# Performance work log

Hardware: AMD Instinct MI355X
Metric: run time of the kernel (lower is better)

Reference implementation:

```python
import jax, jax.numpy as jnp
import numpy as np

B, T, E, H = 2, 2048, 1024, 16
STD = 0.02

def setup_inputs() -> dict:
    key = jax.random.key(0)
    k1, k2, k3 = jax.random.split(key, 3)
    return {
        'x': jax.random.normal(k1, (B, T, E), dtype=jnp.float32),
        'mask': jnp.ones((B, T), dtype=bool),
        'w_attn': jax.random.normal(k2, (E, 3 * E), dtype=jnp.float32) * STD,
        'b_attn': jnp.zeros((3 * E,), dtype=jnp.float32),
        'w_proj': jax.random.normal(k3, (E, E), dtype=jnp.float32) * STD,
        'b_proj': jnp.zeros((E,), dtype=jnp.float32),
    }

def reference(x, mask, w_attn, b_attn, w_proj, b_proj):
    b, t, e = x.shape
    h = H
    hd = e // h  # head_dim
    qkv = x @ w_attn + b_attn                       # [B,T,3E]
    q, k, v = jnp.split(qkv, 3, axis=-1)
    q = q.reshape(b, t, h, hd).transpose(0, 2, 1, 3)  # [B,H,T,hd]
    k = k.reshape(b, t, h, hd).transpose(0, 2, 1, 3)
    v = v.reshape(b, t, h, hd).transpose(0, 2, 1, 3)
    scale = jnp.asarray(hd, dtype=x.dtype) ** (-0.5)
    scores = jnp.einsum('bnth,bnsh->bnts', q, k) * scale  # [B,H,T,T]
    causal = jnp.tril(jnp.ones((t, t), dtype=bool))
    full_mask = causal[None, None, :, :] & mask.astype(bool)[:, None, None, :]
    neg = jnp.asarray(jnp.finfo(x.dtype).min, dtype=x.dtype)
    bias = jnp.where(full_mask, jnp.asarray(0.0, dtype=x.dtype), neg)
    attn = jax.nn.softmax(scores + bias, axis=-1)
    out = jnp.einsum('bnts,bnsh->bnth', attn, v)    # [B,H,T,hd]
    out = out.transpose(0, 2, 1, 3).reshape(b, t, e)
    return out @ w_proj + b_proj
```

## Files before the change

### kernel.cpp

```cpp
#include <hip/hip_runtime.h>

typedef float f32x4 __attribute__((ext_vector_type(4)));
typedef float f32x16 __attribute__((ext_vector_type(16)));
typedef __bf16 bf16x8 __attribute__((ext_vector_type(8)));
typedef unsigned short ushort8_t __attribute__((ext_vector_type(8)));
typedef unsigned short ushort4_t __attribute__((ext_vector_type(4)));

#define GAS(p) ((const __attribute__((address_space(1))) void*)(p))
#define LAS(p) ((__attribute__((address_space(3))) void*)(p))

__device__ inline unsigned short f2bf(float f) {
    union { float f; unsigned int u; } v; v.f = f;
    unsigned int r = v.u + 0x7FFFu + ((v.u >> 16) & 1u);
    return (unsigned short)(r >> 16);
}

__device__ inline bf16x8 ld16(const unsigned short* p) {
    uint4 v = *reinterpret_cast<const uint4*>(p);
    return __builtin_bit_cast(bf16x8, v);
}

__device__ inline unsigned int cvtpk(float a, float b) {
    unsigned int r;
    asm("v_cvt_pk_bf16_f32 %0, %1, %2" : "=v"(r) : "v"(a), "v"(b));
    return r;
}

__device__ inline float swap_max(float x) { return fmaxf(x, __shfl_xor(x, 32)); }
__device__ inline float swap_add(float x) { return x + __shfl_xor(x, 32); }

__global__ __launch_bounds__(256) void k_f32_to_bf16(const float* __restrict__ x,
                                                     unsigned short* __restrict__ y, int n) {
    int i = (blockIdx.x * 256 + threadIdx.x) * 8;
    if (i >= n) return;
    float4 a = *reinterpret_cast<const float4*>(x + i);
    float4 b = *reinterpret_cast<const float4*>(x + i + 4);
    ushort8_t o;
    o[0]=f2bf(a.x); o[1]=f2bf(a.y); o[2]=f2bf(a.z); o[3]=f2bf(a.w);
    o[4]=f2bf(b.x); o[5]=f2bf(b.y); o[6]=f2bf(b.z); o[7]=f2bf(b.w);
    *reinterpret_cast<ushort8_t*>(y + i) = o;
}

__global__ __launch_bounds__(256) void k_transpose_bf16(const float* __restrict__ W,
                                                        unsigned short* __restrict__ WT,
                                                        int K, int N) {
    __shared__ unsigned short tile[64][72];
    int n0 = blockIdx.x * 64, k0 = blockIdx.y * 64;
    int tid = threadIdx.x;
    int r = tid >> 2;
    int c0 = (tid & 3) * 16;
    const float* src = W + (size_t)(k0 + r) * N + n0 + c0;
    #pragma unroll
    for (int i = 0; i < 4; ++i) {
        float4 v = reinterpret_cast<const float4*>(src)[i];
        tile[r][c0 + i*4 + 0] = f2bf(v.x);
        tile[r][c0 + i*4 + 1] = f2bf(v.y);
        tile[r][c0 + i*4 + 2] = f2bf(v.z);
        tile[r][c0 + i*4 + 3] = f2bf(v.w);
    }
    __syncthreads();
    unsigned short tmp[16];
    #pragma unroll
    for (int i = 0; i < 16; ++i) tmp[i] = tile[c0 + i][r];
    unsigned short* dst = WT + (size_t)(n0 + r) * K + k0 + c0;
    ushort8_t o0, o1;
    #pragma unroll
    for (int i = 0; i < 8; ++i) { o0[i] = tmp[i]; o1[i] = tmp[8 + i]; }
    *reinterpret_cast<ushort8_t*>(dst) = o0;
    *reinterpret_cast<ushort8_t*>(dst + 8) = o1;
}

template<int MODE>
__global__ __launch_bounds__(256) void k_gemm(const unsigned short* __restrict__ A,
                                              const unsigned short* __restrict__ BT,
                                              const float* __restrict__ bias,
                                              unsigned short* __restrict__ qo,
                                              unsigned short* __restrict__ ko,
                                              unsigned short* __restrict__ vo,
                                              float* __restrict__ outp,
                                              int K, int N) {
    __shared__ unsigned short As[128 * 32];
    __shared__ unsigned short Bs[128 * 32];
    int tid = threadIdx.x;
    int lane = tid & 63;
    int wave = tid >> 6;
    int wm = wave >> 1, wn = wave & 1;
    int bm = blockIdx.x * 128;
    int bn = blockIdx.y * 128;
    int r15 = lane & 15, g = lane >> 4;

    f32x4 acc[4][4];
    #pragma unroll
    for (int i = 0; i < 4; ++i)
        #pragma unroll
        for (int j = 0; j < 4; ++j)
            acc[i][j] = (f32x4){0.f, 0.f, 0.f, 0.f};

    for (int k0 = 0; k0 < K; k0 += 32) {
        #pragma unroll
        for (int it = 0; it < 2; ++it) {
            int ci = it * 256 + tid;
            int row = ci >> 2, cj = ci & 3;
            const unsigned short* ga = A + (size_t)(bm + row) * K + k0 + cj * 8;
            __builtin_amdgcn_global_load_lds(GAS(ga), LAS(As + (it * 256 + wave * 64) * 8), 16, 0, 0);
            const unsigned short* gb = BT + (size_t)(bn + row) * K + k0 + cj * 8;
            __builtin_amdgcn_global_load_lds(GAS(gb), LAS(Bs + (it * 256 + wave * 64) * 8), 16, 0, 0);
        }
        __syncthreads();
        bf16x8 af[4], bfr[4];
        #pragma unroll
        for (int i = 0; i < 4; ++i) af[i] = ld16(As + (wm * 64 + i * 16 + r15) * 32 + g * 8);
        #pragma unroll
        for (int j = 0; j < 4; ++j) bfr[j] = ld16(Bs + (wn * 64 + j * 16 + r15) * 32 + g * 8);
        #pragma unroll
        for (int i = 0; i < 4; ++i)
            #pragma unroll
            for (int j = 0; j < 4; ++j)
                acc[i][j] = __builtin_amdgcn_mfma_f32_16x16x32_bf16(af[i], bfr[j], acc[i][j], 0, 0, 0);
        __syncthreads();
    }

    const float QSCL = 0.18033688011112042f;
    #pragma unroll
    for (int i = 0; i < 4; ++i)
        #pragma unroll
        for (int j = 0; j < 4; ++j) {
            int col = bn + wn * 64 + j * 16 + r15;
            float bcol = bias[col];
            int row0 = bm + wm * 64 + i * 16 + g * 4;
            if (MODE == 0) {
                int which = col >> 10;
                int e = col & 1023;
                int hh = e >> 6, d = e & 63;
                int bb = row0 >> 11, t0 = row0 & 2047;
                size_t headbase = (size_t)(bb * 16 + hh) * 131072;
                if (which == 2) {
                    int blk = (t0 >> 2) & 3;
                    int t0p = (t0 & ~15) | ((((blk & 1) << 1) | (blk >> 1)) << 2);
                    int tilev = t0p >> 6, s6 = t0p & 63;
                    int sbv = s6 >> 5, s5 = s6 & 31;
                    int ksv = s5 >> 4, hiv = (s5 >> 3) & 1, jb = s5 & 7;
                    int dbv = d >> 5, lanev = hiv * 32 + (d & 31);
                    ushort4_t pk;
                    #pragma unroll
                    for (int rg = 0; rg < 4; ++rg) pk[rg] = f2bf(acc[i][j][rg] + bcol);
                    *reinterpret_cast<ushort4_t*>(vo + headbase +
                        (size_t)((((tilev * 2 + dbv) * 2 + sbv) * 2 + ksv) * 64 + lanev) * 8 + jb) = pk;
                } else {
                    unsigned short* dst = (which == 0) ? qo : ko;
                    float scl = (which == 0) ? QSCL : 1.0f;
                    int grp = t0 >> 5, l31q = t0 & 31;
                    int kbq = d >> 4, hiq = (d >> 3) & 1, jq = d & 7;
                    size_t base = headbase + (size_t)(grp * 4 + kbq) * 512 + hiq * 256 + l31q * 8 + jq;
                    #pragma unroll
                    for (int rg = 0; rg < 4; ++rg)
                        dst[base + rg * 8] = f2bf((acc[i][j][rg] + bcol) * scl);
                }
            } else {
                #pragma unroll
                for (int rg = 0; rg < 4; ++rg)
                    outp[(size_t)(row0 + rg) * 1024 + col] = acc[i][j][rg] + bcol;
            }
        }
}

#define ATTN_HALF(QF, OACC, MM, LL, TR, S0M, MASKED)                           \
  {                                                                            \
    f32x16 sacc[2];                                                            \
    _Pragma("unroll")                                                          \
    for (int sb = 0; sb < 2; ++sb)                                             \
      _Pragma("unroll")                                                        \
      for (int r = 0; r < 16; ++r) sacc[sb][r] = 0.f;                          \
    _Pragma("unroll")                                                          \
    for (int sb = 0; sb < 2; ++sb)                                             \
      _Pragma("unroll")                                                        \
      for (int kb = 0; kb < 4; ++kb)                                           \
        sacc[sb] = __builtin_amdgcn_mfma_f32_32x32x16_bf16(kf[sb][kb], QF[kb], sacc[sb], 0, 0, 0); \
    if (MASKED) {                                                              \
      _Pragma("unroll")                                                        \
      for (int sb = 0; sb < 2; ++sb)                                           \
        _Pragma("unroll")                                                      \
        for (int r = 0; r < 16; ++r) {                                         \
          int srw = (S0M) + sb * 32 + (r & 3) + 8 * (r >> 2) + 4 * hi;         \
          if (srw > (TR)) sacc[sb][r] = -3.0e38f;                              \
        }                                                                      \
    }                                                                          \
    float mt = sacc[0][0];                                                     \
    _Pragma("unroll")                                                          \
    for (int sb = 0; sb < 2; ++sb)                                             \
      _Pragma("unroll")                                                        \
      for (int r = 0; r < 16; ++r) mt = fmaxf(mt, sacc[sb][r]);                \
    mt = swap_max(mt);                                                         \
    if (__any(mt > MM + 8.f)) {                                                \
      float mnew = fmaxf(MM, mt);                                              \
      float alpha = exp2f(MM - mnew);                                          \
      MM = mnew;                                                               \
      LL *= alpha;                                                             \
      _Pragma("unroll")                                                        \
      for (int db = 0; db < 2; ++db)                                           \
        _Pragma("unroll")                                                      \
        for (int r = 0; r < 16; ++r) OACC[db][r] *= alpha;                     \
    }                                                                          \
    float rs = 0.f;                                                            \
    _Pragma("unroll")                                                          \
    for (int sb = 0; sb < 2; ++sb)                                             \
      _Pragma("unroll")                                                        \
      for (int r = 0; r < 16; ++r) {                                           \
        float p = exp2f(sacc[sb][r] - MM);                                     \
        sacc[sb][r] = p;                                                       \
        rs += p;                                                               \
      }                                                                        \
    LL += swap_add(rs);                                                        \
    _Pragma("unroll")                                                          \
    for (int sb = 0; sb < 2; ++sb) {                                           \
      bf16x8 pa[2];                                                            \
      _Pragma("unroll")                                                        \
      for (int ks = 0; ks < 2; ++ks) {                                         \
        int base = ks * 8;                                                     \
        uint4 u;                                                               \
        u.x = cvtpk(sacc[sb][base + 0], sacc[sb][base + 1]);                   \
        u.y = cvtpk(sacc[sb][base + 2], sacc[sb][base + 3]);                   \
        u.z = cvtpk(sacc[sb][base + 4], sacc[sb][base + 5]);                   \
        u.w = cvtpk(sacc[sb][base + 6], sacc[sb][base + 7]);                   \
        pa[ks] = __builtin_bit_cast(bf16x8, u);                                \
      }                                                                        \
      _Pragma("unroll")                                                        \
      for (int db = 0; db < 2; ++db)                                           \
        _Pragma("unroll")                                                      \
        for (int ks = 0; ks < 2; ++ks)                                         \
          OACC[db] = __builtin_amdgcn_mfma_f32_32x32x16_bf16(vf[db][sb][ks], pa[ks], OACC[db], 0, 0, 0); \
    }                                                                          \
  }

#define ATTN_TILE(S0, MASKED)                                                  \
  {                                                                            \
    int s0_ = (S0);                                                            \
    int tg_ = s0_ >> 5;                                                        \
    bf16x8 kf[2][4];                                                           \
    _Pragma("unroll")                                                          \
    for (int sb = 0; sb < 2; ++sb)                                             \
      _Pragma("unroll")                                                        \
      for (int kb = 0; kb < 4; ++kb)                                           \
        kf[sb][kb] = ld16(Kfb + (size_t)((tg_ + sb) * 4 + kb) * 512 + lane * 8); \
    int vt_ = s0_ >> 6;                                                        \
    bf16x8 vf[2][2][2];                                                        \
    _Pragma("unroll")                                                          \
    for (int db = 0; db < 2; ++db)                                             \
      _Pragma("unroll")                                                        \
      for (int sb = 0; sb < 2; ++sb)                                           \
        _Pragma("unroll")                                                      \
        for (int ks = 0; ks < 2; ++ks)                                         \
          vf[db][sb][ks] = ld16(Vfb + (size_t)(((vt_ * 2 + db) * 2 + sb) * 2 + ks) * 512 + lane * 8); \
    ATTN_HALF(qfA, oaccA, mA, lA, trA, s0_, MASKED)                            \
    ATTN_HALF(qfB, oaccB, mB, lB, trB, s0_, MASKED)                            \
  }

#define ATTN_EPI(OACC, LL, ROWBASE)                                            \
  {                                                                            \
    float rl = 1.0f / (LL);                                                    \
    unsigned short* W = Ob[wave];                                              \
    _Pragma("unroll")                                                          \
    for (int db = 0; db < 2; ++db)                                             \
      _Pragma("unroll")                                                        \
      for (int run = 0; run < 4; ++run) {                                      \
        float v0 = OACC[db][run * 4 + 0] * rl;                                 \
        float v1 = OACC[db][run * 4 + 1] * rl;                                 \
        float v2 = OACC[db][run * 4 + 2] * rl;                                 \
        float v3 = OACC[db][run * 4 + 3] * rl;                                 \
        uint2 pk; pk.x = cvtpk(v0, v1); pk.y = cvtpk(v2, v3);                  \
        *reinterpret_cast<uint2*>(&W[l31 * 72 + db * 32 + run * 8 + hi * 4]) = pk; \
      }                                                                        \
    _Pragma("unroll")                                                          \
    for (int it = 0; it < 4; ++it) {                                           \
      int idx2 = it * 64 + lane;                                               \
      int row = idx2 >> 3, ch = idx2 & 7;                                      \
      uint4 v = *reinterpret_cast<const uint4*>(&W[row * 72 + ch * 8]);        \
      *reinterpret_cast<uint4*>(&AO[(size_t)(b * 2048 + (ROWBASE) + row) * 1024 + h * 64 + ch * 8]) = v; \
    }                                                                          \
  }

__global__ __launch_bounds__(128) void k_attn(const unsigned short* __restrict__ Qg,
                                              const unsigned short* __restrict__ Kg,
                                              const unsigned short* __restrict__ VTg,
                                              unsigned short* __restrict__ AO) {
    __shared__ unsigned short Ob[2][32 * 72];
    int tid = threadIdx.x, lane = tid & 63, wave = tid >> 6;
    int l31 = lane & 31, hi = lane >> 5;
    int fb = blockIdx.x;
    int xcd = fb & 7;
    int idx = fb >> 3;
    int bh = xcd + 8 * (idx >> 4);
    int sub = idx & 15;
    int q0 = ((idx & 32) ? sub : (15 - sub)) * 128;
    const unsigned short* Qfb = Qg + (size_t)bh * 131072;
    const unsigned short* Kfb = Kg + (size_t)bh * 131072;
    const unsigned short* Vfb = VTg + (size_t)bh * 131072;
    int qr0 = q0 + wave * 64;
    int trA = qr0 + l31;
    int trB = qr0 + 32 + l31;

    bf16x8 qfA[4], qfB[4];
    #pragma unroll
    for (int kb = 0; kb < 4; ++kb) {
        qfA[kb] = ld16(Qfb + (size_t)((qr0 >> 5) * 4 + kb) * 512 + lane * 8);
        qfB[kb] = ld16(Qfb + (size_t)(((qr0 >> 5) + 1) * 4 + kb) * 512 + lane * 8);
    }

    float mA = -3.0e38f, lA = 0.f, mB = -3.0e38f, lB = 0.f;
    f32x16 oaccA[2], oaccB[2];
    #pragma unroll
    for (int db = 0; db < 2; ++db)
        #pragma unroll
        for (int r = 0; r < 16; ++r) { oaccA[db][r] = 0.f; oaccB[db][r] = 0.f; }

    int NT = (qr0 >> 6) + 1;
    for (int t = 0; t < NT; ++t) ATTN_TILE(t * 64, t == NT - 1)

    int b = bh >> 4, h = bh & 15;
    ATTN_EPI(oaccA, lA, qr0)
    ATTN_EPI(oaccB, lB, qr0 + 32)
}

extern "C" void kernel_launch(void* const* d_in, const int* in_sizes, int n_in,
                              void* d_out, int out_size, void* d_ws, size_t ws_size,
                              hipStream_t stream) {
    (void)in_sizes; (void)n_in; (void)out_size; (void)ws_size;
    const float* x      = (const float*)d_in[0];
    const float* w_attn = (const float*)d_in[2];
    const float* b_attn = (const float*)d_in[3];
    const float* w_proj = (const float*)d_in[4];
    const float* b_proj = (const float*)d_in[5];
    float* out = (float*)d_out;

    unsigned short* xb  = (unsigned short*)d_ws;
    unsigned short* waT = xb  + 4194304;
    unsigned short* wpT = waT + 3145728;
    unsigned short* qb  = wpT + 1048576;
    unsigned short* kb  = qb  + 4194304;
    unsigned short* vTb = kb  + 4194304;
    unsigned short* ao  = vTb + 4194304;

    k_f32_to_bf16<<<2048, 256, 0, stream>>>(x, xb, 4194304);
    k_transpose_bf16<<<dim3(48, 16), 256, 0, stream>>>(w_attn, waT, 1024, 3072);
    k_transpose_bf16<<<dim3(16, 16), 256, 0, stream>>>(w_proj, wpT, 1024, 1024);
    k_gemm<0><<<dim3(32, 24), 256, 0, stream>>>(xb, waT, b_attn, qb, kb, vTb, nullptr, 1024, 3072);
    k_attn<<<512, 128, 0, stream>>>(qb, kb, vTb, ao);
    k_gemm<1><<<dim3(32, 8), 256, 0, stream>>>(ao, wpT, b_proj, nullptr, nullptr, nullptr, out, 1024, 1024);
}
```

Measured before the change: 156.0 us.

## Pair mirrored causal query chunks per wave and tree-reduce softmax max/sum

Each wave now handles two 32-row query chunks, w and 63-w, so every wave does the same total amount of causal work instead of the row-position-dependent load it had before. The tile loop runs to the longer chunk's length and skips the shorter chunk's half once it has finished, with separate mask flags for each chunk. The row max and row sum reductions in the softmax are rewritten as pairwise trees to shorten the dependency chains. The trade-offs are a branch inside the tile loop and K/V fragments being loaded for tiles where only one half does useful work.

```diff
diff --git a/kernel.cpp b/kernel.cpp
--- a/kernel.cpp
+++ b/kernel.cpp
@@ -185,11 +185,14 @@
           if (srw > (TR)) sacc[sb][r] = -3.0e38f;                              \
         }                                                                      \
     }                                                                          \
-    float mt = sacc[0][0];                                                     \
-    _Pragma("unroll")                                                          \
-    for (int sb = 0; sb < 2; ++sb)                                             \
-      _Pragma("unroll")                                                        \
-      for (int r = 0; r < 16; ++r) mt = fmaxf(mt, sacc[sb][r]);                \
+    float tmx[16];                                                             \
+    _Pragma("unroll")                                                          \
+    for (int r = 0; r < 16; ++r) tmx[r] = fmaxf(sacc[0][r], sacc[1][r]);       \
+    _Pragma("unroll")                                                          \
+    for (int r = 0; r < 8; ++r) tmx[r] = fmaxf(tmx[r], tmx[r + 8]);            \
+    _Pragma("unroll")                                                          \
+    for (int r = 0; r < 4; ++r) tmx[r] = fmaxf(tmx[r], tmx[r + 4]);            \
+    float mt = fmaxf(fmaxf(tmx[0], tmx[2]), fmaxf(tmx[1], tmx[3]));            \
     mt = swap_max(mt);                                                         \
     if (__any(mt > MM + 8.f)) {                                                \
       float mnew = fmaxf(MM, mt);                                              \
@@ -201,15 +204,18 @@
         _Pragma("unroll")                                                      \
         for (int r = 0; r < 16; ++r) OACC[db][r] *= alpha;                     \
     }                                                                          \
-    float rs = 0.f;                                                            \
     _Pragma("unroll")                                                          \
     for (int sb = 0; sb < 2; ++sb)                                             \
       _Pragma("unroll")                                                        \
-      for (int r = 0; r < 16; ++r) {                                           \
-        float p = exp2f(sacc[sb][r] - MM);                                     \
-        sacc[sb][r] = p;                                                       \
-        rs += p;                                                               \
-      }                                                                        \
+      for (int r = 0; r < 16; ++r) sacc[sb][r] = exp2f(sacc[sb][r] - MM);      \
+    float tsm[16];                                                             \
+    _Pragma("unroll")                                                          \
+    for (int r = 0; r < 16; ++r) tsm[r] = sacc[0][r] + sacc[1][r];             \
+    _Pragma("unroll")                                                          \
+    for (int r = 0; r < 8; ++r) tsm[r] += tsm[r + 8];                          \
+    _Pragma("unroll")                                                          \
+    for (int r = 0; r < 4; ++r) tsm[r] += tsm[r + 4];                          \
+    float rs = (tsm[0] + tsm[2]) + (tsm[1] + tsm[3]);                          \
     LL += swap_add(rs);                                                        \
     _Pragma("unroll")                                                          \
     for (int sb = 0; sb < 2; ++sb) {                                           \
@@ -232,7 +238,7 @@
     }                                                                          \
   }
 
-#define ATTN_TILE(S0, MASKED)                                                  \
+#define ATTN_TILE(S0, DOA, MA_, MB_)                                           \
   {                                                                            \
     int s0_ = (S0);                                                            \
     int tg_ = s0_ >> 5;                                                        \
@@ -251,8 +257,8 @@
         _Pragma("unroll")                                                      \
         for (int ks = 0; ks < 2; ++ks)                                         \
           vf[db][sb][ks] = ld16(Vfb + (size_t)(((vt_ * 2 + db) * 2 + sb) * 2 + ks) * 512 + lane * 8); \
-    ATTN_HALF(qfA, oaccA, mA, lA, trA, s0_, MASKED)                            \
-    ATTN_HALF(qfB, oaccB, mB, lB, trB, s0_, MASKED)                            \
+    if (DOA) { ATTN_HALF(qfA, oaccA, mA, lA, trA, s0_, MA_) }                  \
+    ATTN_HALF(qfB, oaccB, mB, lB, trB, s0_, MB_)                               \
   }
 
 #define ATTN_EPI(OACC, LL, ROWBASE)                                            \
@@ -290,20 +296,22 @@
     int xcd = fb & 7;
     int idx = fb >> 3;
     int bh = xcd + 8 * (idx >> 4);
-    int sub = idx & 15;
-    int q0 = ((idx & 32) ? sub : (15 - sub)) * 128;
+    int w = (idx & 15) * 2 + wave;
+    int cA = w, cB = 63 - w;
     const unsigned short* Qfb = Qg + (size_t)bh * 131072;
     const unsigned short* Kfb = Kg + (size_t)bh * 131072;
     const unsigned short* Vfb = VTg + (size_t)bh * 131072;
-    int qr0 = q0 + wave * 64;
-    int trA = qr0 + l31;
-    int trB = qr0 + 32 + l31;
+    int qrA = cA * 32, qrB = cB * 32;
+    int trA = qrA + l31;
+    int trB = qrB + l31;
+    int NT_A = (cA >> 1) + 1;
+    int NT_B = (cB >> 1) + 1;
 
     bf16x8 qfA[4], qfB[4];
     #pragma unroll
     for (int kb = 0; kb < 4; ++kb) {
-        qfA[kb] = ld16(Qfb + (size_t)((qr0 >> 5) * 4 + kb) * 512 + lane * 8);
-        qfB[kb] = ld16(Qfb + (size_t)(((qr0 >> 5) + 1) * 4 + kb) * 512 + lane * 8);
+        qfA[kb] = ld16(Qfb + (size_t)(cA * 4 + kb) * 512 + lane * 8);
+        qfB[kb] = ld16(Qfb + (size_t)(cB * 4 + kb) * 512 + lane * 8);
     }
 
     float mA = -3.0e38f, lA = 0.f, mB = -3.0e38f, lB = 0.f;
@@ -313,12 +321,12 @@
         #pragma unroll
         for (int r = 0; r < 16; ++r) { oaccA[db][r] = 0.f; oaccB[db][r] = 0.f; }
 
-    int NT = (qr0 >> 6) + 1;
-    for (int t = 0; t < NT; ++t) ATTN_TILE(t * 64, t == NT - 1)
+    for (int t = 0; t < NT_B; ++t)
+        ATTN_TILE(t * 64, t < NT_A, t == NT_A - 1, t == NT_B - 1)
 
     int b = bh >> 4, h = bh & 15;
-    ATTN_EPI(oaccA, lA, qr0)
-    ATTN_EPI(oaccB, lB, qr0 + 32)
+    ATTN_EPI(oaccA, lA, qrA)
+    ATTN_EPI(oaccB, lB, qrB)
 }
 
 extern "C" void kernel_launch(void* const* d_in, const int* in_sizes, int n_in,
```

Result: faster. 129.0 us (-17.3%).
